# Kernel optimization log

Hardware: AMD Instinct MI355X
Metric: run time of the kernel (lower is better)

## Reference

```python
import jax, jax.numpy as jnp
import numpy as np

B_, T_, TS, DE, H, LD, OD = 16, 4096, 64, 128, 256, 512, 10
RMIN, RMAX, MAXPH = 0.9, 0.999, 6.283
EPS = 1e-5
NBLK = 6


def setup_inputs() -> dict:
    key = jax.random.key(0)
    ks = jax.random.split(key, 14)
    x = jax.random.normal(ks[0], (B_, T_, TS), jnp.float32)
    # LRU ring init (Orvieto et al.)
    u1 = jax.random.uniform(ks[1], (NBLK, H))
    u2 = jax.random.uniform(ks[2], (NBLK, H))
    nu_log = jnp.log(-0.5 * jnp.log(u1 * (RMAX**2 - RMIN**2) + RMIN**2))
    theta_log = jnp.log(MAXPH * u2)
    B_re = jax.random.normal(ks[3], (NBLK, H, DE)) / np.sqrt(2 * DE)
    B_im = jax.random.normal(ks[4], (NBLK, H, DE)) / np.sqrt(2 * DE)
    C_re = jax.random.normal(ks[5], (NBLK, DE, H)) / np.sqrt(H)
    C_im = jax.random.normal(ks[6], (NBLK, DE, H)) / np.sqrt(H)
    D_lru = jax.random.normal(ks[7], (NBLK, DE))
    W1 = jax.random.normal(ks[8], (NBLK, DE, LD)) / np.sqrt(DE)
    b1 = jnp.zeros((NBLK, LD))
    W2 = jax.random.normal(ks[9], (NBLK, LD // 2, DE)) / np.sqrt(LD // 2)
    b2 = jnp.zeros((NBLK, DE))
    bn_scale = jnp.ones((NBLK, DE))
    bn_bias = jnp.zeros((NBLK, DE))
    W_enc = jax.random.normal(ks[10], (TS, DE)) / np.sqrt(TS)
    b_enc = jnp.zeros((DE,))
    W_out = jax.random.normal(ks[11], (DE, OD)) / np.sqrt(DE)
    b_out = jnp.zeros((OD,))
    return dict(x=x, nu_log=nu_log, theta_log=theta_log, B_re=B_re, B_im=B_im,
                C_re=C_re, C_im=C_im, D_lru=D_lru, W1=W1, b1=b1, W2=W2, b2=b2,
                bn_scale=bn_scale, bn_bias=bn_bias, W_enc=W_enc, b_enc=b_enc,
                W_out=W_out, b_out=b_out)


def _lru(u, nu_log_i, theta_log_i, Bre, Bim, Cre, Cim, Dv):
    # u: [B,T,DE] float. Diagonal complex linear recurrence via associative scan.
    lam = jnp.exp(-jnp.exp(nu_log_i) + 1j * jnp.exp(theta_log_i))        # [H]
    gamma = jnp.sqrt(jnp.clip(1.0 - jnp.abs(lam) ** 2, 1e-8, None))      # [H]
    Bc = (Bre + 1j * Bim) * gamma[:, None]                               # [H,DE]
    Bu = jnp.einsum('btd,hd->bth', u.astype(jnp.complex64), Bc)          # [B,T,H]
    lam_b = jnp.broadcast_to(lam, Bu.shape)

    def binop(a, b):
        return (a[0] * b[0], a[1] * b[0] + b[1])

    _, h = jax.lax.associative_scan(binop, (lam_b, Bu), axis=1)          # [B,T,H]
    y = jnp.einsum('bth,dh->btd', h, Cre + 1j * Cim).real + u * Dv
    return y


def _bn(x, scale, bias):
    # training-mode batchnorm over (batch, time) with feature axis last
    m = x.mean(axis=(0, 1))
    v = x.var(axis=(0, 1))
    return (x - m) * jax.lax.rsqrt(v + EPS) * scale + bias


def reference(x, nu_log, theta_log, B_re, B_im, C_re, C_im, D_lru,
              W1, b1, W2, b2, bn_scale, bn_bias, W_enc, b_enc, W_out, b_out):
    h = x @ W_enc + b_enc                       # [B,T,DE]
    y = h
    for i in range(NBLK):
        z = _bn(h, bn_scale[i], bn_bias[i])
        z = _lru(z, nu_log[i], theta_log[i], B_re[i], B_im[i], C_re[i], C_im[i], D_lru[i])
        z = z @ W1[i] + b1[i]                   # [B,T,LD]
        a, b = jnp.split(z, 2, axis=-1)
        z = a * jax.nn.sigmoid(b)               # GLU
        z = z @ W2[i] + b2[i]                   # [B,T,DE]
        h = z + y                               # residual to encoder output
    pooled = h.mean(axis=1)                     # pool=True: mean over tokens
    return pooled @ W_out + b_out               # [B,OD]
```

## Files before the change

kernel.cpp:

```cpp
#include <hip/hip_runtime.h>
#include <hip/hip_fp16.h>

#define BB 16
#define TT 4096
#define TSZ 64
#define DE 128
#define HH 256
#define LDIM 512
#define ODIM 10
#define NBLKS 6
#define EPSF 1e-5f
#define NC32 128
#define NROWS (BB*TT)

typedef _Float16 f16x8 __attribute__((ext_vector_type(8)));
typedef _Float16 f16x4 __attribute__((ext_vector_type(4)));
typedef float f32x4 __attribute__((ext_vector_type(4)));
#define MFMA16(a,b,c) __builtin_amdgcn_mfma_f32_16x16x32_f16((a),(b),(c),0,0,0)

enum : size_t {
  HOFF_BG = 0,
  HOFF_WC = HOFF_BG + (size_t)NBLKS*512*128,
  HOFF_W1 = HOFF_WC + (size_t)NBLKS*128*512,
  HOFF_W2 = HOFF_W1 + (size_t)NBLKS*512*128,
  HOFF_WE = HOFF_W2 + (size_t)NBLKS*128*256,
  HTOT_HALFS = HOFF_WE + 128*64
};

enum : size_t {
  WOFF_Y     = 0,
  WOFF_H     = WOFF_Y + (size_t)NROWS*DE/2,
  WOFF_W16   = WOFF_H + (size_t)NROWS*DE/2,
  WOFF_LAM   = WOFF_W16 + (HTOT_HALFS+1)/2,
  WOFF_LAML  = WOFF_LAM + (size_t)NBLKS*HH*2,
  WOFF_SL    = WOFF_LAML + (size_t)NBLKS*HH*2,
  WOFF_CARRY = WOFF_SL + (size_t)BB*NC32*HH*2,
  WOFF_STATS = WOFF_CARRY + (size_t)BB*NC32*HH*2,
  WOFF_POOL  = WOFF_STATS + (size_t)(NBLKS+1)*2*DE,
  WOFF_BU    = WOFF_POOL + (size_t)BB*DE,
  WS_FLOATS  = WOFF_BU + (size_t)BB*NC32*512*32/2
};

__global__ __launch_bounds__(256) void k_prep(
    const float* __restrict__ nu_log, const float* __restrict__ theta_log,
    const float* __restrict__ B_re, const float* __restrict__ B_im,
    const float* __restrict__ C_re, const float* __restrict__ C_im,
    const float* __restrict__ W1g, const float* __restrict__ W2g,
    const float* __restrict__ Wenc, float* __restrict__ ws)
{
  const int i = blockIdx.x, h = threadIdx.x;
  __half* w16 = (__half*)(ws + WOFF_W16);
  const float nu  = expf(nu_log[i*HH+h]);
  const float th  = expf(theta_log[i*HH+h]);
  const float mod = expf(-nu);
  const float lr = mod*cosf(th), li = mod*sinf(th);
  const float gamma = sqrtf(fmaxf(1.0f - mod*mod, 1e-8f));
  ws[WOFF_LAM + ((size_t)i*HH+h)*2+0] = lr;
  ws[WOFF_LAM + ((size_t)i*HH+h)*2+1] = li;
  {
    float ar = lr, ai = li;
    #pragma unroll
    for (int q = 0; q < 5; q++) { float nr=ar*ar-ai*ai, ni=2.0f*ar*ai; ar=nr; ai=ni; }
    ws[WOFF_LAML + ((size_t)i*HH+h)*2+0] = ar;
    ws[WOFF_LAML + ((size_t)i*HH+h)*2+1] = ai;
  }
  {
    __half* bg = w16 + HOFF_BG + (size_t)i*512*128;
    const float* bre = B_re + ((size_t)i*HH+h)*DE;
    const float* bim = B_im + ((size_t)i*HH+h)*DE;
    for (int d = 0; d < DE; d++) {
      bg[(size_t)h*128 + d]       = __float2half(bre[d]*gamma);
      bg[(size_t)(256+h)*128 + d] = __float2half(bim[d]*gamma);
    }
  }
  {
    __half* wc = w16 + HOFF_WC + (size_t)i*128*512;
    const float* cre = C_re + (size_t)i*DE*HH;
    const float* cim = C_im + (size_t)i*DE*HH;
    for (int d = 0; d < DE; d++) {
      wc[(size_t)d*512 + 2*h]     = __float2half( cre[(size_t)d*HH + h]);
      wc[(size_t)d*512 + 2*h + 1] = __float2half(-cim[(size_t)d*HH + h]);
    }
  }
  {
    __half* w1t = w16 + HOFF_W1 + (size_t)i*512*128;
    for (int d = 0; d < DE; d++) {
      w1t[(size_t)h*128 + d]       = __float2half(W1g[((size_t)i*DE + d)*LDIM + h]);
      w1t[(size_t)(256+h)*128 + d] = __float2half(W1g[((size_t)i*DE + d)*LDIM + 256 + h]);
    }
  }
  if (h < 128) {
    __half* w2t = w16 + HOFF_W2 + (size_t)i*128*256;
    for (int g = 0; g < 256; g++)
      w2t[(size_t)h*256 + g] = __float2half(W2g[((size_t)i*256 + g)*DE + h]);
  }
  if (i == 0 && h < 128) {
    __half* wet = w16 + HOFF_WE;
    for (int k = 0; k < TSZ; k++)
      wet[(size_t)h*TSZ + k] = __float2half(Wenc[(size_t)k*DE + h]);
  }
}

__global__ __launch_bounds__(512) void k_enc(
    const float* __restrict__ x, const float* __restrict__ benc, float* __restrict__ ws)
{
  __shared__ __half XT[64*72];
  __shared__ __half YS[64*136];
  const int tid = threadIdx.x, w = tid >> 6, l = tid & 63;
  const size_t row0 = (size_t)blockIdx.x * 64;
  {
    const float4* xg = (const float4*)(x + row0*TSZ);
    for (int idx = tid; idx < 1024; idx += 512) {
      float4 v = xg[idx];
      const int r = idx >> 4, c4 = (idx & 15)*4;
      *(__half2*)&XT[r*72 + c4]     = __half2{__float2half(v.x), __float2half(v.y)};
      *(__half2*)&XT[r*72 + c4 + 2] = __half2{__float2half(v.z), __float2half(v.w)};
    }
  }
  __syncthreads();
  const __half* wet = (const __half*)(ws + WOFF_W16) + HOFF_WE;
  const int n0 = w*16;
  f32x4 acc[4];
  #pragma unroll
  for (int mt = 0; mt < 4; mt++) acc[mt] = (f32x4)(0.0f);
  #pragma unroll
  for (int k0 = 0; k0 < 64; k0 += 32) {
    f16x8 bf = *(const f16x8*)&wet[(size_t)(n0 + (l&15))*64 + k0 + (l>>4)*8];
    #pragma unroll
    for (int mt = 0; mt < 4; mt++) {
      f16x8 af = *(const f16x8*)&XT[(mt*16 + (l&15))*72 + k0 + (l>>4)*8];
      acc[mt] = MFMA16(af, bf, acc[mt]);
    }
  }
  const int d = n0 + (l&15);
  const float be = benc[d];
  float s = 0.0f, ss = 0.0f;
  #pragma unroll
  for (int mt = 0; mt < 4; mt++)
    #pragma unroll
    for (int j = 0; j < 4; j++) {
      const int t = mt*16 + (l>>4)*4 + j;
      const float v = acc[mt][j] + be;
      YS[t*136 + d] = __float2half(v);
      s += v; ss += v*v;
    }
  s  += __shfl_xor(s, 16);  s  += __shfl_xor(s, 32);
  ss += __shfl_xor(ss, 16); ss += __shfl_xor(ss, 32);
  if (l < 16) {
    atomicAdd(ws + WOFF_STATS + d, s);
    atomicAdd(ws + WOFF_STATS + DE + d, ss);
  }
  __syncthreads();
  __half* y = (__half*)(ws + WOFF_Y);
  const int row = tid >> 3, d0 = (tid & 7)*16;
  *(f16x8*)&y[(row0+row)*DE + d0]     = *(const f16x8*)&YS[row*136 + d0];
  *(f16x8*)&y[(row0+row)*DE + d0 + 8] = *(const f16x8*)&YS[row*136 + d0 + 8];
}

__global__ __launch_bounds__(512, 4) void k_A(
    const __half* __restrict__ hin, float* __restrict__ ws,
    const float* __restrict__ bnsg, const float* __restrict__ bnbg, int iblk)
{
  __shared__ __half U[32*136];
  __shared__ __half BU[32*520];
  __shared__ float AC[256];
  const int tid = threadIdx.x, w = tid >> 6, l = tid & 63, q = l >> 4, r = l & 15;
  const int b = blockIdx.y, cbg = blockIdx.x;
  const int h = tid & 255;
  if (tid < 128) {
    const float inv = 1.0f / (float)NROWS;
    const float s  = ws[WOFF_STATS + ((size_t)iblk*2+0)*DE + tid];
    const float sq = ws[WOFF_STATS + ((size_t)iblk*2+1)*DE + tid];
    const float mean = s*inv;
    const float var  = sq*inv - mean*mean;
    const float a = rsqrtf(var + EPSF) * bnsg[iblk*DE + tid];
    AC[tid]       = a;
    AC[128 + tid] = bnbg[iblk*DE + tid] - mean*a;
  }
  const __half* BG = (const __half*)(ws + WOFF_W16) + HOFF_BG + (size_t)iblk*512*128;
  const int n0 = w*64;
  const float lr = ws[WOFF_LAM + ((size_t)iblk*HH+h)*2+0];
  const float li = ws[WOFF_LAM + ((size_t)iblk*HH+h)*2+1];
  f16x8 bg4[4][4];
  #pragma unroll
  for (int nt = 0; nt < 4; nt++)
    #pragma unroll
    for (int k = 0; k < 4; k++)
      bg4[nt][k] = *(const f16x8*)&BG[(size_t)(n0 + nt*16 + r)*128 + k*32 + q*8];
  __half* bug = (__half*)(ws + WOFF_BU);
  __syncthreads();

  for (int it = 0; it < 4; it++) {
    const int cb = cbg*4 + it;
    const int row0 = b*TT + cb*32;
    {
      const int row = tid >> 4, d0 = (tid & 15)*8;
      f16x8 hv = *(const f16x8*)(hin + (size_t)(row0+row)*DE + d0);
      f16x8 uv;
      #pragma unroll
      for (int j = 0; j < 8; j++)
        uv[j] = (_Float16)((float)hv[j]*AC[d0+j] + AC[128+d0+j]);
      *(f16x8*)&U[row*136 + d0] = uv;
    }
    __syncthreads();
    {
      f32x4 acc[2][4];
      #pragma unroll
      for (int mt = 0; mt < 2; mt++)
        #pragma unroll
        for (int nt = 0; nt < 4; nt++) acc[mt][nt] = (f32x4)(0.0f);
      #pragma unroll
      for (int k = 0; k < 4; k++) {
        f16x8 af0 = *(const f16x8*)&U[(r)*136      + k*32 + q*8];
        f16x8 af1 = *(const f16x8*)&U[(16 + r)*136 + k*32 + q*8];
        #pragma unroll
        for (int nt = 0; nt < 4; nt++) {
          acc[0][nt] = MFMA16(af0, bg4[nt][k], acc[0][nt]);
          acc[1][nt] = MFMA16(af1, bg4[nt][k], acc[1][nt]);
        }
      }
      #pragma unroll
      for (int mt = 0; mt < 2; mt++)
        #pragma unroll
        for (int nt = 0; nt < 4; nt++) {
          f16x4 pk;
          #pragma unroll
          for (int j = 0; j < 4; j++) {
            pk[j] = (_Float16)acc[mt][nt][j];
            BU[(mt*16 + q*4 + j)*520 + n0 + nt*16 + r] = __float2half(acc[mt][nt][j]);
          }
          const int hc = n0 + nt*16 + r;
          *(f16x4*)(bug + (((size_t)(b*NC32 + cb)*512 + hc)*32 + mt*16 + q*4)) = pk;
        }
    }
    __syncthreads();
    if (tid < 256) {
      float sr = 0.0f, si = 0.0f;
      #pragma unroll
      for (int t = 0; t < 32; t++) {
        const float br = (float)BU[t*520 + h];
        const float bi = (float)BU[t*520 + 256 + h];
        const float nr = lr*sr - li*si + br;
        const float ni = lr*si + li*sr + bi;
        sr = nr; si = ni;
      }
      *((float2*)(ws + WOFF_SL) + ((size_t)b*NC32 + cb)*HH + h) = float2{sr, si};
    }
    __syncthreads();
  }
}

__global__ void k_carry(float* __restrict__ ws, int i)
{
  const int b = blockIdx.x >> 2;
  const int h = (blockIdx.x & 3)*64 + threadIdx.x;
  const float Lr = ws[WOFF_LAML + ((size_t)i*HH+h)*2+0];
  const float Li = ws[WOFF_LAML + ((size_t)i*HH+h)*2+1];
  float2* C = (float2*)(ws + WOFF_CARRY) + (size_t)b*NC32*HH + h;
  const float2* S = (const float2*)(ws + WOFF_SL) + (size_t)b*NC32*HH + h;
  float sr = 0.0f, si = 0.0f;
  C[0] = float2{0.0f, 0.0f};
  for (int c0 = 0; c0 < 120; c0 += 8) {
    float2 sl[8];
    #pragma unroll
    for (int j = 0; j < 8; j++) sl[j] = S[(size_t)(c0+j)*HH];
    #pragma unroll
    for (int j = 0; j < 8; j++) {
      const float nr = Lr*sr - Li*si + sl[j].x;
      const float ni = Lr*si + Li*sr + sl[j].y;
      sr = nr; si = ni;
      C[(size_t)(c0+j+1)*HH] = float2{sr, si};
    }
  }
  {
    float2 sl[7];
    #pragma unroll
    for (int j = 0; j < 7; j++) sl[j] = S[(size_t)(120+j)*HH];
    #pragma unroll
    for (int j = 0; j < 7; j++) {
      const float nr = Lr*sr - Li*si + sl[j].x;
      const float ni = Lr*si + Li*sr + sl[j].y;
      sr = nr; si = ni;
      C[(size_t)(121+j)*HH] = float2{sr, si};
    }
  }
}

__global__ __launch_bounds__(512, 4) void k_BC(
    const __half* __restrict__ hin, float* __restrict__ ws,
    const float* __restrict__ bnsg, const float* __restrict__ bnbg,
    const float* __restrict__ b1g, const float* __restrict__ b2g,
    const float* __restrict__ Dvg, int iblk, int islast)
{
  __shared__ __half U[32*136];
  __shared__ __half HT[32*520];
  __shared__ __half YL[32*136];
  __shared__ __half YR[32*136];
  __shared__ float AC[256];
  __shared__ float DVs[128];
  const int tid = threadIdx.x, w = tid >> 6, l = tid & 63, q = l >> 4, r = l & 15;
  const int b = blockIdx.y, cbg = blockIdx.x;
  const __half* w16 = (const __half*)(ws + WOFF_W16);
  const int d = w*16 + r;
  const int h = tid & 255;

  if (tid < 128) {
    const float inv = 1.0f / (float)NROWS;
    const float s  = ws[WOFF_STATS + ((size_t)iblk*2+0)*DE + tid];
    const float sq = ws[WOFF_STATS + ((size_t)iblk*2+1)*DE + tid];
    const float mean = s*inv;
    const float var  = sq*inv - mean*mean;
    const float a = rsqrtf(var + EPSF) * bnsg[iblk*DE + tid];
    AC[tid]       = a;
    AC[128 + tid] = bnbg[iblk*DE + tid] - mean*a;
    DVs[tid] = Dvg[iblk*DE + tid];
  }

  const float lr = ws[WOFF_LAM + ((size_t)iblk*HH+h)*2+0];
  const float li = ws[WOFF_LAM + ((size_t)iblk*HH+h)*2+1];
  float b1a[2], b1b[2];
  #pragma unroll
  for (int nt = 0; nt < 2; nt++) {
    const int ca = w*32 + nt*16 + r;
    b1a[nt] = b1g[(size_t)iblk*LDIM + ca];
    b1b[nt] = b1g[(size_t)iblk*LDIM + 256 + ca];
  }
  const float bb2 = b2g[(size_t)iblk*DE + d];
  const __half* WC  = w16 + HOFF_WC + (size_t)iblk*128*512;
  const __half* W1T = w16 + HOFF_W1 + (size_t)iblk*512*128;
  const __half* W2T = w16 + HOFF_W2 + (size_t)iblk*128*256;
  const __half* bug = (const __half*)(ws + WOFF_BU);
  const __half* yh = (const __half*)(ws + WOFF_Y);
  __half* hh = (__half*)(ws + WOFF_H);
  float s_acc = 0.0f, ss_acc = 0.0f;
  __syncthreads();

  for (int it = 0; it < 4; it++) {
    const int cb = cbg*4 + it;
    const int row0 = b*TT + cb*32;

    {
      const int row = tid >> 4, d0 = (tid & 15)*8;
      f16x8 hv  = *(const f16x8*)(hin + (size_t)(row0+row)*DE + d0);
      f16x8 yv8 = *(const f16x8*)(yh  + (size_t)(row0+row)*DE + d0);
      f16x8 uv;
      #pragma unroll
      for (int j = 0; j < 8; j++)
        uv[j] = (_Float16)((float)hv[j]*AC[d0+j] + AC[128+d0+j]);
      *(f16x8*)&U[row*136 + d0]  = uv;
      *(f16x8*)&YR[row*136 + d0] = yv8;
    }
    if (tid < 256) {
      const __half* bu = bug + ((size_t)(b*NC32 + cb)*512)*32;
      f16x8 bre[4], bim[4];
      #pragma unroll
      for (int k = 0; k < 4; k++) {
        bre[k] = *(const f16x8*)(bu + (size_t)h*32 + k*8);
        bim[k] = *(const f16x8*)(bu + (size_t)(256+h)*32 + k*8);
      }
      const float2 carry = *((const float2*)(ws + WOFF_CARRY) + ((size_t)b*NC32 + cb)*HH + h);
      float sr = carry.x, si = carry.y;
      #pragma unroll
      for (int t = 0; t < 32; t++) {
        const float br = (float)bre[t>>3][t&7];
        const float bi = (float)bim[t>>3][t&7];
        const float nr = lr*sr - li*si + br;
        const float ni = lr*si + li*sr + bi;
        sr = nr; si = ni;
        *(__half2*)&HT[t*520 + 2*h] = __half2{__float2half(sr), __float2half(si)};
      }
    }
    __syncthreads();

    {
      f16x8 wc[16];
      #pragma unroll
      for (int k = 0; k < 16; k++)
        wc[k] = *(const f16x8*)&WC[(size_t)d*512 + k*32 + q*8];
      f32x4 a0 = (f32x4)(0.0f), a1 = (f32x4)(0.0f);
      #pragma unroll
      for (int k = 0; k < 16; k++) {
        f16x8 af0 = *(const f16x8*)&HT[(r)*520      + k*32 + q*8];
        f16x8 af1 = *(const f16x8*)&HT[(16 + r)*520 + k*32 + q*8];
        a0 = MFMA16(af0, wc[k], a0);
        a1 = MFMA16(af1, wc[k], a1);
      }
      const float dv = DVs[d];
      #pragma unroll
      for (int mt = 0; mt < 2; mt++)
        #pragma unroll
        for (int j = 0; j < 4; j++) {
          const int t = mt*16 + q*4 + j;
          const float u = (float)U[t*136 + d];
          YL[t*136 + d] = __float2half((mt ? a1[j] : a0[j]) + u*dv);
        }
    }
    __syncthreads();

    {
      #pragma unroll
      for (int nt = 0; nt < 2; nt++) {
        const int ca = w*32 + nt*16 + r;
        f16x8 wa[4], wb[4];
        #pragma unroll
        for (int k = 0; k < 4; k++) {
          wa[k] = *(const f16x8*)&W1T[(size_t)ca*128 + k*32 + q*8];
          wb[k] = *(const f16x8*)&W1T[(size_t)(256+ca)*128 + k*32 + q*8];
        }
        f32x4 aa0 = (f32x4)(0.0f), aa1 = (f32x4)(0.0f);
        f32x4 ab0 = (f32x4)(0.0f), ab1 = (f32x4)(0.0f);
        #pragma unroll
        for (int k = 0; k < 4; k++) {
          f16x8 af0 = *(const f16x8*)&YL[(r)*136      + k*32 + q*8];
          f16x8 af1 = *(const f16x8*)&YL[(16 + r)*136 + k*32 + q*8];
          aa0 = MFMA16(af0, wa[k], aa0);
          aa1 = MFMA16(af1, wa[k], aa1);
          ab0 = MFMA16(af0, wb[k], ab0);
          ab1 = MFMA16(af1, wb[k], ab1);
        }
        #pragma unroll
        for (int mt = 0; mt < 2; mt++)
          #pragma unroll
          for (int j = 0; j < 4; j++) {
            const int t = mt*16 + q*4 + j;
            const float av = (mt ? aa1[j] : aa0[j]) + b1a[nt];
            const float bv = (mt ? ab1[j] : ab0[j]) + b1b[nt];
            HT[t*520 + ca] = __float2half(av / (1.0f + __expf(-bv)));
          }
      }
    }
    __syncthreads();

    {
      f16x8 w2f[8];
      #pragma unroll
      for (int k = 0; k < 8; k++)
        w2f[k] = *(const f16x8*)&W2T[(size_t)d*256 + k*32 + q*8];
      f32x4 a0 = (f32x4)(0.0f), a1 = (f32x4)(0.0f);
      #pragma unroll
      for (int k = 0; k < 8; k++) {
        f16x8 af0 = *(const f16x8*)&HT[(r)*520      + k*32 + q*8];
        f16x8 af1 = *(const f16x8*)&HT[(16 + r)*520 + k*32 + q*8];
        a0 = MFMA16(af0, w2f[k], a0);
        a1 = MFMA16(af1, w2f[k], a1);
      }
      #pragma unroll
      for (int mt = 0; mt < 2; mt++)
        #pragma unroll
        for (int j = 0; j < 4; j++) {
          const int t = mt*16 + q*4 + j;
          const float v = (mt ? a1[j] : a0[j]) + bb2 + (float)YR[t*136 + d];
          YR[t*136 + d] = __float2half(v);
          s_acc += v; ss_acc += v*v;
        }
    }
    __syncthreads();

    {
      const int row = tid >> 4, d0 = (tid & 15)*8;
      *(f16x8*)(hh + (size_t)(row0+row)*DE + d0) = *(const f16x8*)&YR[row*136 + d0];
    }
    __syncthreads();
  }

  s_acc  += __shfl_xor(s_acc, 16);  s_acc  += __shfl_xor(s_acc, 32);
  ss_acc += __shfl_xor(ss_acc, 16); ss_acc += __shfl_xor(ss_acc, 32);
  if (l < 16) {
    atomicAdd(ws + WOFF_STATS + (size_t)((iblk+1)*2 + 0)*DE + d, s_acc);
    atomicAdd(ws + WOFF_STATS + (size_t)((iblk+1)*2 + 1)*DE + d, ss_acc);
    if (islast) atomicAdd(ws + WOFF_POOL + (size_t)b*DE + d, s_acc);
  }
}

__global__ void k_out(const float* __restrict__ Wout, const float* __restrict__ bout,
                      const float* __restrict__ ws, float* __restrict__ out)
{
  const int tid = threadIdx.x;
  if (tid < BB*ODIM) {
    const int b = tid / ODIM, o = tid % ODIM;
    float acc = bout[o];
    const float* p = ws + WOFF_POOL + (size_t)b*DE;
    const float invT = 1.0f / (float)TT;
    for (int d = 0; d < DE; d++) acc += p[d]*invT*Wout[d*ODIM + o];
    out[tid] = acc;
  }
}

extern "C" void kernel_launch(void* const* d_in, const int* in_sizes, int n_in,
                              void* d_out, int out_size, void* d_ws, size_t ws_size,
                              hipStream_t stream)
{
  const float* x   = (const float*)d_in[0];
  const float* nu  = (const float*)d_in[1];
  const float* th  = (const float*)d_in[2];
  const float* Bre = (const float*)d_in[3];
  const float* Bim = (const float*)d_in[4];
  const float* Cre = (const float*)d_in[5];
  const float* Cim = (const float*)d_in[6];
  const float* Dv  = (const float*)d_in[7];
  const float* W1  = (const float*)d_in[8];
  const float* b1  = (const float*)d_in[9];
  const float* W2  = (const float*)d_in[10];
  const float* b2  = (const float*)d_in[11];
  const float* bns = (const float*)d_in[12];
  const float* bnb = (const float*)d_in[13];
  const float* We  = (const float*)d_in[14];
  const float* be  = (const float*)d_in[15];
  const float* Wo  = (const float*)d_in[16];
  const float* bo  = (const float*)d_in[17];
  float* ws = (float*)d_ws;
  float* out = (float*)d_out;

  hipMemsetAsync(ws + WOFF_STATS, 0,
                 (size_t)(((NBLKS+1)*2*DE) + BB*DE)*sizeof(float), stream);

  k_prep<<<NBLKS, 256, 0, stream>>>(nu, th, Bre, Bim, Cre, Cim, W1, W2, We, ws);
  k_enc<<<NROWS/64, 512, 0, stream>>>(x, be, ws);

  const __half* Yh = (const __half*)(ws + WOFF_Y);
  const __half* Hh = (const __half*)(ws + WOFF_H);
  for (int i = 0; i < NBLKS; i++) {
    const __half* hin = (i == 0) ? Yh : Hh;
    k_A    <<<dim3(32, BB), 512, 0, stream>>>(hin, ws, bns, bnb, i);
    k_carry<<<64, 64, 0, stream>>>(ws, i);
    k_BC   <<<dim3(32, BB), 512, 0, stream>>>(hin, ws, bns, bnb, b1, b2, Dv, i,
                                              (i == NBLKS-1) ? 1 : 0);
  }
  k_out<<<1, 256, 0, stream>>>(Wo, bo, ws, out);
}
```

Measured before the change: 901.0 us.

## Parallelize weight prep, double grid for scan kernels, cut LDS in k_BC

k_prep now runs on a 2D grid, each block converting an 8-column slice with vectorized half stores instead of one block looping over all columns. k_A and k_BC launch twice as many blocks, each handling 2 chunks instead of 4. k_BC drops the YL/YR shared buffers by reusing HT and U, changes the WC/HT layout from interleaved re/im to split halves, and raises occupancy to 6 waves per SIMD. BU padding goes from 520 to 536 to reduce bank conflicts. Risks include register pressure under the tighter launch bounds and a WC layout change that must match the split HT layout.

```diff
diff --git a/kernel.cpp b/kernel.cpp
--- a/kernel.cpp
+++ b/kernel.cpp
@@ -48,56 +48,76 @@
     const float* __restrict__ W1g, const float* __restrict__ W2g,
     const float* __restrict__ Wenc, float* __restrict__ ws)
 {
-  const int i = blockIdx.x, h = threadIdx.x;
+  const int i = blockIdx.x, s = blockIdx.y, h = threadIdx.x;
   __half* w16 = (__half*)(ws + WOFF_W16);
   const float nu  = expf(nu_log[i*HH+h]);
   const float th  = expf(theta_log[i*HH+h]);
   const float mod = expf(-nu);
-  const float lr = mod*cosf(th), li = mod*sinf(th);
   const float gamma = sqrtf(fmaxf(1.0f - mod*mod, 1e-8f));
-  ws[WOFF_LAM + ((size_t)i*HH+h)*2+0] = lr;
-  ws[WOFF_LAM + ((size_t)i*HH+h)*2+1] = li;
-  {
+
+  if (s == 0) {
+    const float lr = mod*cosf(th), li = mod*sinf(th);
+    ws[WOFF_LAM + ((size_t)i*HH+h)*2+0] = lr;
+    ws[WOFF_LAM + ((size_t)i*HH+h)*2+1] = li;
     float ar = lr, ai = li;
     #pragma unroll
     for (int q = 0; q < 5; q++) { float nr=ar*ar-ai*ai, ni=2.0f*ar*ai; ar=nr; ai=ni; }
     ws[WOFF_LAML + ((size_t)i*HH+h)*2+0] = ar;
     ws[WOFF_LAML + ((size_t)i*HH+h)*2+1] = ai;
-  }
+    if (i == 0 && h < 128) {
+      __half* wet = w16 + HOFF_WE;
+      for (int k = 0; k < TSZ; k++)
+        wet[(size_t)h*TSZ + k] = __float2half(Wenc[(size_t)k*DE + h]);
+    }
+  }
+
+  const int d0 = s*8;
   {
     __half* bg = w16 + HOFF_BG + (size_t)i*512*128;
-    const float* bre = B_re + ((size_t)i*HH+h)*DE;
-    const float* bim = B_im + ((size_t)i*HH+h)*DE;
-    for (int d = 0; d < DE; d++) {
-      bg[(size_t)h*128 + d]       = __float2half(bre[d]*gamma);
-      bg[(size_t)(256+h)*128 + d] = __float2half(bim[d]*gamma);
-    }
+    const float* bre = B_re + ((size_t)i*HH+h)*DE + d0;
+    const float* bim = B_im + ((size_t)i*HH+h)*DE + d0;
+    f16x8 vr, vi;
+    #pragma unroll
+    for (int j = 0; j < 8; j++) {
+      vr[j] = (_Float16)(bre[j]*gamma);
+      vi[j] = (_Float16)(bim[j]*gamma);
+    }
+    *(f16x8*)&bg[(size_t)h*128 + d0]       = vr;
+    *(f16x8*)&bg[(size_t)(256+h)*128 + d0] = vi;
   }
   {
     __half* wc = w16 + HOFF_WC + (size_t)i*128*512;
     const float* cre = C_re + (size_t)i*DE*HH;
     const float* cim = C_im + (size_t)i*DE*HH;
-    for (int d = 0; d < DE; d++) {
-      wc[(size_t)d*512 + 2*h]     = __float2half( cre[(size_t)d*HH + h]);
-      wc[(size_t)d*512 + 2*h + 1] = __float2half(-cim[(size_t)d*HH + h]);
+    #pragma unroll
+    for (int j = 0; j < 8; j++) {
+      const int d = d0 + j;
+      wc[(size_t)d*512 + h]       = __float2half( cre[(size_t)d*HH + h]);
+      wc[(size_t)d*512 + 256 + h] = __float2half(-cim[(size_t)d*HH + h]);
     }
   }
   {
     __half* w1t = w16 + HOFF_W1 + (size_t)i*512*128;
-    for (int d = 0; d < DE; d++) {
-      w1t[(size_t)h*128 + d]       = __float2half(W1g[((size_t)i*DE + d)*LDIM + h]);
-      w1t[(size_t)(256+h)*128 + d] = __float2half(W1g[((size_t)i*DE + d)*LDIM + 256 + h]);
-    }
+    f16x8 v0, v1;
+    #pragma unroll
+    for (int j = 0; j < 8; j++) {
+      v0[j] = (_Float16)W1g[((size_t)i*DE + d0 + j)*LDIM + h];
+      v1[j] = (_Float16)W1g[((size_t)i*DE + d0 + j)*LDIM + 256 + h];
+    }
+    *(f16x8*)&w1t[(size_t)h*128 + d0]       = v0;
+    *(f16x8*)&w1t[(size_t)(256+h)*128 + d0] = v1;
   }
   if (h < 128) {
     __half* w2t = w16 + HOFF_W2 + (size_t)i*128*256;
-    for (int g = 0; g < 256; g++)
-      w2t[(size_t)h*256 + g] = __float2half(W2g[((size_t)i*256 + g)*DE + h]);
-  }
-  if (i == 0 && h < 128) {
-    __half* wet = w16 + HOFF_WE;
-    for (int k = 0; k < TSZ; k++)
-      wet[(size_t)h*TSZ + k] = __float2half(Wenc[(size_t)k*DE + h]);
+    const int g0 = s*16;
+    f16x8 v0, v1;
+    #pragma unroll
+    for (int j = 0; j < 8; j++) {
+      v0[j] = (_Float16)W2g[((size_t)i*256 + g0 + j)*DE + h];
+      v1[j] = (_Float16)W2g[((size_t)i*256 + g0 + 8 + j)*DE + h];
+    }
+    *(f16x8*)&w2t[(size_t)h*256 + g0]     = v0;
+    *(f16x8*)&w2t[(size_t)h*256 + g0 + 8] = v1;
   }
 }
 
@@ -162,7 +182,7 @@
     const float* __restrict__ bnsg, const float* __restrict__ bnbg, int iblk)
 {
   __shared__ __half U[32*136];
-  __shared__ __half BU[32*520];
+  __shared__ __half BU[32*536];
   __shared__ float AC[256];
   const int tid = threadIdx.x, w = tid >> 6, l = tid & 63, q = l >> 4, r = l & 15;
   const int b = blockIdx.y, cbg = blockIdx.x;
@@ -190,8 +210,8 @@
   __half* bug = (__half*)(ws + WOFF_BU);
   __syncthreads();
 
-  for (int it = 0; it < 4; it++) {
-    const int cb = cbg*4 + it;
+  for (int it = 0; it < 2; it++) {
+    const int cb = cbg*2 + it;
     const int row0 = b*TT + cb*32;
     {
       const int row = tid >> 4, d0 = (tid & 15)*8;
@@ -227,7 +247,7 @@
           #pragma unroll
           for (int j = 0; j < 4; j++) {
             pk[j] = (_Float16)acc[mt][nt][j];
-            BU[(mt*16 + q*4 + j)*520 + n0 + nt*16 + r] = __float2half(acc[mt][nt][j]);
+            BU[(mt*16 + q*4 + j)*536 + n0 + nt*16 + r] = __float2half(acc[mt][nt][j]);
           }
           const int hc = n0 + nt*16 + r;
           *(f16x4*)(bug + (((size_t)(b*NC32 + cb)*512 + hc)*32 + mt*16 + q*4)) = pk;
@@ -238,8 +258,8 @@
       float sr = 0.0f, si = 0.0f;
       #pragma unroll
       for (int t = 0; t < 32; t++) {
-        const float br = (float)BU[t*520 + h];
-        const float bi = (float)BU[t*520 + 256 + h];
+        const float br = (float)BU[t*536 + h];
+        const float bi = (float)BU[t*536 + 256 + h];
         const float nr = lr*sr - li*si + br;
         const float ni = lr*si + li*sr + bi;
         sr = nr; si = ni;
@@ -286,7 +306,7 @@
   }
 }
 
-__global__ __launch_bounds__(512, 4) void k_BC(
+__global__ __launch_bounds__(512, 6) void k_BC(
     const __half* __restrict__ hin, float* __restrict__ ws,
     const float* __restrict__ bnsg, const float* __restrict__ bnbg,
     const float* __restrict__ b1g, const float* __restrict__ b2g,
@@ -294,8 +314,6 @@
 {
   __shared__ __half U[32*136];
   __shared__ __half HT[32*520];
-  __shared__ __half YL[32*136];
-  __shared__ __half YR[32*136];
   __shared__ float AC[256];
   __shared__ float DVs[128];
   const int tid = threadIdx.x, w = tid >> 6, l = tid & 63, q = l >> 4, r = l & 15;
@@ -335,20 +353,18 @@
   float s_acc = 0.0f, ss_acc = 0.0f;
   __syncthreads();
 
-  for (int it = 0; it < 4; it++) {
-    const int cb = cbg*4 + it;
+  for (int it = 0; it < 2; it++) {
+    const int cb = cbg*2 + it;
     const int row0 = b*TT + cb*32;
 
     {
       const int row = tid >> 4, d0 = (tid & 15)*8;
-      f16x8 hv  = *(const f16x8*)(hin + (size_t)(row0+row)*DE + d0);
-      f16x8 yv8 = *(const f16x8*)(yh  + (size_t)(row0+row)*DE + d0);
+      f16x8 hv = *(const f16x8*)(hin + (size_t)(row0+row)*DE + d0);
       f16x8 uv;
       #pragma unroll
       for (int j = 0; j < 8; j++)
         uv[j] = (_Float16)((float)hv[j]*AC[d0+j] + AC[128+d0+j]);
-      *(f16x8*)&U[row*136 + d0]  = uv;
-      *(f16x8*)&YR[row*136 + d0] = yv8;
+      *(f16x8*)&U[row*136 + d0] = uv;
     }
     if (tid < 256) {
       const __half* bu = bug + ((size_t)(b*NC32 + cb)*512)*32;
@@ -367,23 +383,28 @@
         const float nr = lr*sr - li*si + br;
         const float ni = lr*si + li*sr + bi;
         sr = nr; si = ni;
-        *(__half2*)&HT[t*520 + 2*h] = __half2{__float2half(sr), __float2half(si)};
-      }
-    }
-    __syncthreads();
-
-    {
-      f16x8 wc[16];
-      #pragma unroll
-      for (int k = 0; k < 16; k++)
-        wc[k] = *(const f16x8*)&WC[(size_t)d*512 + k*32 + q*8];
+        HT[t*520 + h]       = __float2half(sr);
+        HT[t*520 + 256 + h] = __float2half(si);
+      }
+    }
+    __syncthreads();
+
+    float ylv[2][4];
+    {
       f32x4 a0 = (f32x4)(0.0f), a1 = (f32x4)(0.0f);
       #pragma unroll
-      for (int k = 0; k < 16; k++) {
-        f16x8 af0 = *(const f16x8*)&HT[(r)*520      + k*32 + q*8];
-        f16x8 af1 = *(const f16x8*)&HT[(16 + r)*520 + k*32 + q*8];
-        a0 = MFMA16(af0, wc[k], a0);
-        a1 = MFMA16(af1, wc[k], a1);
+      for (int kb = 0; kb < 2; kb++) {
+        f16x8 wc[8];
+        #pragma unroll
+        for (int k = 0; k < 8; k++)
+          wc[k] = *(const f16x8*)&WC[(size_t)d*512 + kb*256 + k*32 + q*8];
+        #pragma unroll
+        for (int k = 0; k < 8; k++) {
+          f16x8 af0 = *(const f16x8*)&HT[(r)*520      + kb*256 + k*32 + q*8];
+          f16x8 af1 = *(const f16x8*)&HT[(16 + r)*520 + kb*256 + k*32 + q*8];
+          a0 = MFMA16(af0, wc[k], a0);
+          a1 = MFMA16(af1, wc[k], a1);
+        }
       }
       const float dv = DVs[d];
       #pragma unroll
@@ -392,42 +413,51 @@
         for (int j = 0; j < 4; j++) {
           const int t = mt*16 + q*4 + j;
           const float u = (float)U[t*136 + d];
-          YL[t*136 + d] = __float2half((mt ? a1[j] : a0[j]) + u*dv);
+          ylv[mt][j] = (mt ? a1[j] : a0[j]) + u*dv;
         }
     }
     __syncthreads();
 
-    {
-      #pragma unroll
-      for (int nt = 0; nt < 2; nt++) {
-        const int ca = w*32 + nt*16 + r;
-        f16x8 wa[4], wb[4];
-        #pragma unroll
-        for (int k = 0; k < 4; k++) {
-          wa[k] = *(const f16x8*)&W1T[(size_t)ca*128 + k*32 + q*8];
-          wb[k] = *(const f16x8*)&W1T[(size_t)(256+ca)*128 + k*32 + q*8];
+    #pragma unroll
+    for (int mt = 0; mt < 2; mt++)
+      #pragma unroll
+      for (int j = 0; j < 4; j++)
+        HT[(mt*16 + q*4 + j)*520 + 256 + d] = __float2half(ylv[mt][j]);
+    {
+      const int row = tid >> 4, d0 = (tid & 15)*8;
+      *(f16x8*)&U[row*136 + d0] = *(const f16x8*)(yh + (size_t)(row0+row)*DE + d0);
+    }
+    __syncthreads();
+
+    #pragma unroll
+    for (int nt = 0; nt < 2; nt++) {
+      const int ca = w*32 + nt*16 + r;
+      f16x8 wa[4], wb[4];
+      #pragma unroll
+      for (int k = 0; k < 4; k++) {
+        wa[k] = *(const f16x8*)&W1T[(size_t)ca*128 + k*32 + q*8];
+        wb[k] = *(const f16x8*)&W1T[(size_t)(256+ca)*128 + k*32 + q*8];
+      }
+      f32x4 aa0 = (f32x4)(0.0f), aa1 = (f32x4)(0.0f);
+      f32x4 ab0 = (f32x4)(0.0f), ab1 = (f32x4)(0.0f);
+      #pragma unroll
+      for (int k = 0; k < 4; k++) {
+        f16x8 af0 = *(const f16x8*)&HT[(r)*520      + 256 + k*32 + q*8];
+        f16x8 af1 = *(const f16x8*)&HT[(16 + r)*520 + 256 + k*32 + q*8];
+        aa0 = MFMA16(af0, wa[k], aa0);
+        aa1 = MFMA16(af1, wa[k], aa1);
+        ab0 = MFMA16(af0, wb[k], ab0);
+        ab1 = MFMA16(af1, wb[k], ab1);
+      }
+      #pragma unroll
+      for (int mt = 0; mt < 2; mt++)
+        #pragma unroll
+        for (int j = 0; j < 4; j++) {
+          const int t = mt*16 + q*4 + j;
+          const float av = (mt ? aa1[j] : aa0[j]) + b1a[nt];
+          const float bv = (mt ? ab1[j] : ab0[j]) + b1b[nt];
+          HT[t*520 + ca] = __float2half(av / (1.0f + __expf(-bv)));
         }
-        f32x4 aa0 = (f32x4)(0.0f), aa1 = (f32x4)(0.0f);
-        f32x4 ab0 = (f32x4)(0.0f), ab1 = (f32x4)(0.0f);
-        #pragma unroll
-        for (int k = 0; k < 4; k++) {
-          f16x8 af0 = *(const f16x8*)&YL[(r)*136      + k*32 + q*8];
-          f16x8 af1 = *(const f16x8*)&YL[(16 + r)*136 + k*32 + q*8];
-          aa0 = MFMA16(af0, wa[k], aa0);
-          aa1 = MFMA16(af1, wa[k], aa1);
-          ab0 = MFMA16(af0, wb[k], ab0);
-          ab1 = MFMA16(af1, wb[k], ab1);
-        }
-        #pragma unroll
-        for (int mt = 0; mt < 2; mt++)
-          #pragma unroll
-          for (int j = 0; j < 4; j++) {
-            const int t = mt*16 + q*4 + j;
-            const float av = (mt ? aa1[j] : aa0[j]) + b1a[nt];
-            const float bv = (mt ? ab1[j] : ab0[j]) + b1b[nt];
-            HT[t*520 + ca] = __float2half(av / (1.0f + __expf(-bv)));
-          }
-      }
     }
     __syncthreads();
 
@@ -449,8 +479,8 @@
         #pragma unroll
         for (int j = 0; j < 4; j++) {
           const int t = mt*16 + q*4 + j;
-          const float v = (mt ? a1[j] : a0[j]) + bb2 + (float)YR[t*136 + d];
-          YR[t*136 + d] = __float2half(v);
+          const float v = (mt ? a1[j] : a0[j]) + bb2 + (float)U[t*136 + d];
+          U[t*136 + d] = __float2half(v);
           s_acc += v; ss_acc += v*v;
         }
     }
@@ -458,7 +488,7 @@
 
     {
       const int row = tid >> 4, d0 = (tid & 15)*8;
-      *(f16x8*)(hh + (size_t)(row0+row)*DE + d0) = *(const f16x8*)&YR[row*136 + d0];
+      *(f16x8*)(hh + (size_t)(row0+row)*DE + d0) = *(const f16x8*)&U[row*136 + d0];
     }
     __syncthreads();
   }
@@ -514,16 +544,16 @@
   hipMemsetAsync(ws + WOFF_STATS, 0,
                  (size_t)(((NBLKS+1)*2*DE) + BB*DE)*sizeof(float), stream);
 
-  k_prep<<<NBLKS, 256, 0, stream>>>(nu, th, Bre, Bim, Cre, Cim, W1, W2, We, ws);
+  k_prep<<<dim3(NBLKS, 16), 256, 0, stream>>>(nu, th, Bre, Bim, Cre, Cim, W1, W2, We, ws);
   k_enc<<<NROWS/64, 512, 0, stream>>>(x, be, ws);
 
   const __half* Yh = (const __half*)(ws + WOFF_Y);
   const __half* Hh = (const __half*)(ws + WOFF_H);
   for (int i = 0; i < NBLKS; i++) {
     const __half* hin = (i == 0) ? Yh : Hh;
-    k_A    <<<dim3(32, BB), 512, 0, stream>>>(hin, ws, bns, bnb, i);
+    k_A    <<<dim3(64, BB), 512, 0, stream>>>(hin, ws, bns, bnb, i);
     k_carry<<<64, 64, 0, stream>>>(ws, i);
-    k_BC   <<<dim3(32, BB), 512, 0, stream>>>(hin, ws, bns, bnb, b1, b2, Dv, i,
+    k_BC   <<<dim3(64, BB), 512, 0, stream>>>(hin, ws, bns, bnb, b1, b2, Dv, i,
                                               (i == NBLKS-1) ? 1 : 0);
   }
   k_out<<<1, 256, 0, stream>>>(Wo, bo, ws, out);
```

After: 951.2 us. 1.06x slower.
